# Performance work log

Hardware: AMD Instinct MI355X
Metric: run time of the kernel (lower is better)

Reference implementation:

```python
import jax, jax.numpy as jnp
import numpy as np

PS = 7        # patch (window) size
DIM = 192     # channels
HEADS = 8
HID = 768     # mlp hidden = 4*dim
B = 8
HH = 112
WW = 112
EPS = 1e-5


def _rel_pos_index(ps):
    coords = np.stack(np.meshgrid(np.arange(ps), np.arange(ps), indexing='ij'))
    cf = coords.reshape(2, -1)
    rel = (cf[:, :, None] - cf[:, None, :]).transpose(1, 2, 0).astype(np.int64)
    rel[:, :, 0] += ps - 1
    rel[:, :, 1] += ps - 1
    rel[:, :, 0] *= 2 * ps - 1
    return rel.sum(-1)  # (N, N)

REL_IDX = jnp.asarray(_rel_pos_index(PS))  # (49, 49) int


def layer_norm(x, g, b):
    m = jnp.mean(x, axis=-1, keepdims=True)
    v = jnp.var(x, axis=-1, keepdims=True)
    return (x - m) * jax.lax.rsqrt(v + EPS) * g + b


def setup_inputs() -> dict:
    key = jax.random.key(0)
    ks = jax.random.split(key, 8)
    s = 0.02
    return {
        'x': jax.random.normal(ks[0], (B, HH * WW, DIM), jnp.float32),
        'norm1_g': jnp.ones((DIM,), jnp.float32),
        'norm1_b': jnp.zeros((DIM,), jnp.float32),
        'q_w': jax.random.normal(ks[1], (DIM, DIM), jnp.float32) * s,
        'q_b': jnp.zeros((DIM,), jnp.float32),
        'kv_w': jax.random.normal(ks[2], (2 * DIM, DIM), jnp.float32) * s,
        'kv_b': jnp.zeros((2 * DIM,), jnp.float32),
        'rpe_table': jax.random.normal(ks[3], ((2 * PS - 1) ** 2, HEADS), jnp.float32) * s,
        'proj_w': jax.random.normal(ks[4], (DIM, DIM), jnp.float32) * s,
        'proj_b': jnp.zeros((DIM,), jnp.float32),
        'norm2_g': jnp.ones((DIM,), jnp.float32),
        'norm2_b': jnp.zeros((DIM,), jnp.float32),
        'fc1_w': jax.random.normal(ks[5], (HID, DIM), jnp.float32) * s,
        'fc1_b': jnp.zeros((HID,), jnp.float32),
        'dw_w': jax.random.normal(ks[6], (HID, 1, 3, 3), jnp.float32) * s,
        'dw_b': jnp.zeros((HID,), jnp.float32),
        'fc2_w': jax.random.normal(ks[7], (DIM, HID), jnp.float32) * s,
        'fc2_b': jnp.zeros((DIM,), jnp.float32),
        'H': HH,
        'W': WW,
    }


def reference(x, norm1_g, norm1_b, q_w, q_b, kv_w, kv_b, rpe_table,
              proj_w, proj_b, norm2_g, norm2_b, fc1_w, fc1_b, dw_w, dw_b,
              fc2_w, fc2_b, H, W):
    Bsz, L, C = x.shape
    N = PS * PS
    hd = C // HEADS
    scale = hd ** -0.5
    nh, nw = H // PS, W // PS  # H, W chosen divisible by PS -> no padding

    shortcut = x
    xn = layer_norm(x, norm1_g, norm1_b)
    xi = xn.reshape(Bsz, H, W, C)
    # partition into non-overlapping PS x PS windows: (B*nP, N, C)
    p = xi.reshape(Bsz, nh, PS, nw, PS, C).transpose(0, 1, 3, 2, 4, 5).reshape(-1, N, C)

    # IPSA window attention (memory == x, T = 1)
    q = (p @ q_w.T + q_b).reshape(-1, N, HEADS, hd).transpose(0, 2, 1, 3) * scale
    kv = (p @ kv_w.T + kv_b).reshape(-1, N, 2, HEADS, hd).transpose(2, 0, 3, 1, 4)
    k, v = kv[0], kv[1]  # (B_, heads, N, hd)
    attn = jnp.einsum('bhnd,bhmd->bhnm', q, k)
    bias = rpe_table[REL_IDX.reshape(-1)].reshape(N, N, HEADS).transpose(2, 0, 1)
    attn = jax.nn.softmax(attn + bias[None], axis=-1)
    out = jnp.einsum('bhnm,bhmd->bhnd', attn, v).transpose(0, 2, 1, 3).reshape(-1, N, C)
    out = out @ proj_w.T + proj_b
    # reverse window partition back to (B, L, C)
    out = out.reshape(Bsz, nh, nw, PS, PS, C).transpose(0, 1, 3, 2, 4, 5).reshape(Bsz, L, C)
    x = shortcut + out

    # MLP with depthwise conv
    y = layer_norm(x, norm2_g, norm2_b)
    y = y @ fc1_w.T + fc1_b  # (B, L, HID)
    yc = y.transpose(0, 2, 1).reshape(Bsz, HID, H, W)
    yc = jax.lax.conv_general_dilated(
        yc, dw_w, window_strides=(1, 1), padding=((1, 1), (1, 1)),
        dimension_numbers=('NCHW', 'OIHW', 'NCHW'), feature_group_count=HID,
    ) + dw_b[None, :, None, None]
    y = yc.reshape(Bsz, HID, L).transpose(0, 2, 1)
    y = jax.nn.gelu(y, approximate=False)
    y = y @ fc2_w.T + fc2_b
    return x + y
```

## Files before the change

kernel.cpp:

```cpp
#include <hip/hip_runtime.h>
#include <hip/hip_bf16.h>
#include <cmath>

#define C_DIM 192
#define HID 768

typedef __attribute__((ext_vector_type(8))) __bf16 bf16x8;
typedef __attribute__((ext_vector_type(4))) float f32x4;
typedef __attribute__((ext_vector_type(2))) float f32x2;

__device__ __forceinline__ void gload_lds16(const void* g, void* l) {
  __builtin_amdgcn_global_load_lds(
      (__attribute__((address_space(1))) void*)(const_cast<void*>(g)),
      (__attribute__((address_space(3))) void*)(l), 16, 0, 0);
}

__device__ __forceinline__ float bfu2f(ushort u) {
  return __uint_as_float((unsigned)u << 16);
}
__device__ __forceinline__ ushort f2bfu(float f) {
  __hip_bfloat16 h = __float2bfloat16(f);
  return *reinterpret_cast<ushort*>(&h);
}
__device__ __forceinline__ float fgelu(float x) {
  float z = x * (1.5957691216f + 0.071354816f * x * x);
  return x / (1.f + __expf(-z));
}

__global__ __launch_bounds__(256) void prep_kernel(
    const float* __restrict__ q_w, const float* __restrict__ q_b,
    const float* __restrict__ kv_w, const float* __restrict__ kv_b,
    const float* __restrict__ proj_w, const float* __restrict__ fc1_w,
    const float* __restrict__ fc2_w,
    __hip_bfloat16* __restrict__ wcat, float* __restrict__ bcat,
    __hip_bfloat16* __restrict__ projw, __hip_bfloat16* __restrict__ fc1w,
    __hip_bfloat16* __restrict__ fc2w)
{
  int idx = blockIdx.x * 256 + threadIdx.x;
  const float scale = 0.20412414523193154f;
  if (idx < 110592) {
    float v = (idx < 36864) ? q_w[idx] * scale : kv_w[idx - 36864];
    wcat[idx] = __float2bfloat16(v);
  }
  if (idx < 576) bcat[idx] = (idx < 192) ? q_b[idx] * scale : kv_b[idx - 192];
  if (idx < 36864) projw[idx] = __float2bfloat16(proj_w[idx]);
  if (idx < 147456) {
    fc1w[idx] = __float2bfloat16(fc1_w[idx]);
    fc2w[idx] = __float2bfloat16(fc2_w[idx]);
  }
}

__global__ __launch_bounds__(256) void ln_kernel(
    const float* __restrict__ x, const float* __restrict__ g,
    const float* __restrict__ b, __hip_bfloat16* __restrict__ out)
{
  int t = blockIdx.x * 4 + (threadIdx.x >> 6);
  int lane = threadIdx.x & 63;
  const float* xr = x + (size_t)t * C_DIM;
  float v0 = xr[lane], v1 = xr[lane + 64], v2 = xr[lane + 128];
  float s = v0 + v1 + v2;
  float sq = v0 * v0 + v1 * v1 + v2 * v2;
  #pragma unroll
  for (int off = 32; off > 0; off >>= 1) {
    s += __shfl_xor(s, off, 64);
    sq += __shfl_xor(sq, off, 64);
  }
  float mean = s * (1.0f / 192.0f);
  float var = sq * (1.0f / 192.0f) - mean * mean;
  float rstd = rsqrtf(var + 1e-5f);
  size_t o = (size_t)t * C_DIM;
  out[o + lane]       = __float2bfloat16((v0 - mean) * rstd * g[lane] + b[lane]);
  out[o + lane + 64]  = __float2bfloat16((v1 - mean) * rstd * g[lane + 64] + b[lane + 64]);
  out[o + lane + 128] = __float2bfloat16((v2 - mean) * rstd * g[lane + 128] + b[lane + 128]);
}

template <int EPI>
__global__ __launch_bounds__(512, 4) void gemmA_kernel(
    const ushort* __restrict__ X, int lda, const ushort* __restrict__ W,
    const float* __restrict__ bias, const float* __restrict__ addin,
    void* __restrict__ outp, int N)
{
  __shared__ __align__(16) ushort Al[128 * 192];
  __shared__ __align__(16) ushort Bl[64 * 192];
  const int tid = threadIdx.x;
  const int wv = tid >> 6;
  const int lane = tid & 63;
  const int quad = lane >> 4;
  const int m15 = lane & 15;
  const long mBase = (long)blockIdx.y * 128;
  const int NT = N >> 6;

  #pragma unroll
  for (int r = 0; r < 6; ++r) {
    int sI = tid + r * 512;
    int row = sI / 24;
    int cs = sI - row * 24;
    int gc = cs - (row % 24); if (gc < 0) gc += 24;
    gload_lds16(X + (mBase + row) * (long)lda + gc * 8, Al + sI * 8);
  }

  const int rA0 = wv * 16 + m15;
  const int rA0m = rA0 % 24;

  for (int nt = 0; nt < NT; ++nt) {
    __syncthreads();
    #pragma unroll
    for (int r = 0; r < 3; ++r) {
      int sI = tid + r * 512;
      int row = sI / 24;
      int cs = sI - row * 24;
      int gc = cs - (row % 24); if (gc < 0) gc += 24;
      gload_lds16(W + (long)(nt * 64 + row) * 192 + gc * 8, Bl + sI * 8);
    }
    __syncthreads();

    f32x4 acc[4];
    #pragma unroll
    for (int c = 0; c < 4; ++c) acc[c] = (f32x4){0.f, 0.f, 0.f, 0.f};

    #pragma unroll
    for (int ks = 0; ks < 6; ++ks) {
      const int l = ks * 4 + quad;
      int pa0 = l + rA0m; if (pa0 >= 24) pa0 -= 24;
      bf16x8 a0 = *(const bf16x8*)&Al[rA0 * 192 + pa0 * 8];
      #pragma unroll
      for (int ct = 0; ct < 4; ++ct) {
        const int rB = ct * 16 + m15;
        int pb = l + (rB % 24); if (pb >= 24) pb -= 24;
        bf16x8 b = *(const bf16x8*)&Bl[rB * 192 + pb * 8];
        acc[ct] = __builtin_amdgcn_mfma_f32_16x16x32_bf16(a0, b, acc[ct], 0, 0, 0);
      }
    }
    #pragma unroll
    for (int ct = 0; ct < 4; ++ct)
      #pragma unroll
      for (int i = 0; i < 4; ++i) {
        long row = mBase + wv * 16 + quad * 4 + i;
        int col = nt * 64 + ct * 16 + m15;
        float v = acc[ct][i] + bias[col];
        if (EPI == 1) {
          v += addin[row * N + col];
          ((float*)outp)[row * N + col] = v;
        } else {
          ((__hip_bfloat16*)outp)[row * N + col] = __float2bfloat16(v);
        }
      }
  }
}

__global__ __launch_bounds__(512, 4) void gemmA_ln_kernel(
    const ushort* __restrict__ X, int lda, const ushort* __restrict__ W,
    const float* __restrict__ bias, const float* __restrict__ addin,
    float* __restrict__ outp, const float* __restrict__ lng,
    const float* __restrict__ lnb, __hip_bfloat16* __restrict__ xnout)
{
  __shared__ __align__(16) ushort Al[128 * 192];
  __shared__ __align__(16) ushort Bl[64 * 192];
  const int tid = threadIdx.x;
  const int wv = tid >> 6;
  const int lane = tid & 63;
  const int quad = lane >> 4;
  const int m15 = lane & 15;
  const long mBase = (long)blockIdx.y * 128;

  #pragma unroll
  for (int r = 0; r < 6; ++r) {
    int sI = tid + r * 512;
    int row = sI / 24;
    int cs = sI - row * 24;
    int gc = cs - (row % 24); if (gc < 0) gc += 24;
    gload_lds16(X + (mBase + row) * (long)lda + gc * 8, Al + sI * 8);
  }

  const int rA0 = wv * 16 + m15;
  const int rA0m = rA0 % 24;

  f32x4 acc[3][4];
  #pragma unroll
  for (int n = 0; n < 3; ++n)
    #pragma unroll
    for (int c = 0; c < 4; ++c) acc[n][c] = (f32x4){0.f, 0.f, 0.f, 0.f};

  #pragma unroll
  for (int nt = 0; nt < 3; ++nt) {
    __syncthreads();
    #pragma unroll
    for (int r = 0; r < 3; ++r) {
      int sI = tid + r * 512;
      int row = sI / 24;
      int cs = sI - row * 24;
      int gc = cs - (row % 24); if (gc < 0) gc += 24;
      gload_lds16(W + (long)(nt * 64 + row) * 192 + gc * 8, Bl + sI * 8);
    }
    __syncthreads();
    #pragma unroll
    for (int ks = 0; ks < 6; ++ks) {
      const int l = ks * 4 + quad;
      int pa0 = l + rA0m; if (pa0 >= 24) pa0 -= 24;
      bf16x8 a0 = *(const bf16x8*)&Al[rA0 * 192 + pa0 * 8];
      #pragma unroll
      for (int ct = 0; ct < 4; ++ct) {
        const int rB = ct * 16 + m15;
        int pb = l + (rB % 24); if (pb >= 24) pb -= 24;
        bf16x8 b = *(const bf16x8*)&Bl[rB * 192 + pb * 8];
        acc[nt][ct] = __builtin_amdgcn_mfma_f32_16x16x32_bf16(a0, b, acc[nt][ct], 0, 0, 0);
      }
    }
  }

  float sum_[4], sq_[4];
  #pragma unroll
  for (int i = 0; i < 4; ++i) { sum_[i] = 0.f; sq_[i] = 0.f; }

  #pragma unroll
  for (int nt = 0; nt < 3; ++nt)
    #pragma unroll
    for (int ct = 0; ct < 4; ++ct) {
      int col = nt * 64 + ct * 16 + m15;
      float cb = bias[col];
      #pragma unroll
      for (int i = 0; i < 4; ++i) {
        long row = mBase + wv * 16 + quad * 4 + i;
        float v = acc[nt][ct][i] + cb + addin[row * 192 + col];
        outp[row * 192 + col] = v;
        acc[nt][ct][i] = v;
        sum_[i] += v;
        sq_[i] += v * v;
      }
    }

  float mean_[4], rstd_[4];
  #pragma unroll
  for (int i = 0; i < 4; ++i) {
    float s = sum_[i], q = sq_[i];
    #pragma unroll
    for (int m = 1; m < 16; m <<= 1) {
      s += __shfl_xor(s, m, 64);
      q += __shfl_xor(q, m, 64);
    }
    float mean = s * (1.0f / 192.0f);
    mean_[i] = mean;
    rstd_[i] = rsqrtf(q * (1.0f / 192.0f) - mean * mean + 1e-5f);
  }

  #pragma unroll
  for (int nt = 0; nt < 3; ++nt)
    #pragma unroll
    for (int ct = 0; ct < 4; ++ct) {
      int col = nt * 64 + ct * 16 + m15;
      float cg = lng[col], cbb = lnb[col];
      #pragma unroll
      for (int i = 0; i < 4; ++i) {
        long row = mBase + wv * 16 + quad * 4 + i;
        float v = (acc[nt][ct][i] - mean_[i]) * rstd_[i] * cg + cbb;
        xnout[row * 192 + col] = __float2bfloat16(v);
      }
    }
}

__global__ __launch_bounds__(512, 4) void gemmB_kernel(
    const ushort* __restrict__ X, const ushort* __restrict__ W,
    const float* __restrict__ bias, const float* __restrict__ addin,
    float* __restrict__ outp)
{
  __shared__ __align__(16) ushort Al[128 * 192];
  __shared__ __align__(16) ushort Bl[64 * 192];
  const int tid = threadIdx.x;
  const int wv = tid >> 6;
  const int lane = tid & 63;
  const int quad = lane >> 4;
  const int m15 = lane & 15;
  const long mBase = (long)blockIdx.y * 128;

  const int rA0 = wv * 16 + m15;
  const int rA0m = rA0 % 24;

  f32x4 acc[3][4];
  #pragma unroll
  for (int n = 0; n < 3; ++n)
    #pragma unroll
    for (int c = 0; c < 4; ++c) acc[n][c] = (f32x4){0.f, 0.f, 0.f, 0.f};

  for (int kc = 0; kc < 4; ++kc) {
    for (int nt = 0; nt < 3; ++nt) {
      __syncthreads();
      if (nt == 0) {
        #pragma unroll
        for (int r = 0; r < 6; ++r) {
          int sI = tid + r * 512;
          int row = sI / 24;
          int cs = sI - row * 24;
          int gc = cs - (row % 24); if (gc < 0) gc += 24;
          gload_lds16(X + (mBase + row) * 768l + kc * 192 + gc * 8, Al + sI * 8);
        }
      }
      #pragma unroll
      for (int r = 0; r < 3; ++r) {
        int sI = tid + r * 512;
        int row = sI / 24;
        int cs = sI - row * 24;
        int gc = cs - (row % 24); if (gc < 0) gc += 24;
        gload_lds16(W + (long)(nt * 64 + row) * 768 + kc * 192 + gc * 8, Bl + sI * 8);
      }
      __syncthreads();
      #pragma unroll
      for (int ks = 0; ks < 6; ++ks) {
        const int l = ks * 4 + quad;
        int pa0 = l + rA0m; if (pa0 >= 24) pa0 -= 24;
        bf16x8 a0 = *(const bf16x8*)&Al[rA0 * 192 + pa0 * 8];
        #pragma unroll
        for (int ct = 0; ct < 4; ++ct) {
          const int rB = ct * 16 + m15;
          int pb = l + (rB % 24); if (pb >= 24) pb -= 24;
          bf16x8 b = *(const bf16x8*)&Bl[rB * 192 + pb * 8];
          acc[nt][ct] = __builtin_amdgcn_mfma_f32_16x16x32_bf16(a0, b, acc[nt][ct], 0, 0, 0);
        }
      }
    }
  }
  #pragma unroll
  for (int nt = 0; nt < 3; ++nt)
    #pragma unroll
    for (int ct = 0; ct < 4; ++ct)
      #pragma unroll
      for (int i = 0; i < 4; ++i) {
        long row = mBase + wv * 16 + quad * 4 + i;
        int col = nt * 64 + ct * 16 + m15;
        float v = acc[nt][ct][i] + bias[col] + addin[row * 192 + col];
        outp[row * 192 + col] = v;
      }
}

__global__ __launch_bounds__(256) void attn_kernel(
    const float* __restrict__ rpe, __hip_bfloat16* __restrict__ qkv)
{
  __shared__ float lds[4 * 2352 + 4 * 172];
  const int tid = threadIdx.x;
  const int lane = tid & 63;
  const int wv = tid >> 6;
  const int wh = blockIdx.x * 4 + wv;
  const int h = wh & 7;
  const int win = wh >> 3;
  const int b = win >> 8;
  const int wl = win & 255;
  const int whi = wl >> 4;
  const int wwi = wl & 15;
  ushort* qkv_u = (ushort*)qkv;
  float* kv_w = &lds[wv * 2352];
  float* bias_w = &lds[4 * 2352 + wv * 172];

  const long rowbase = (long)b * 12544 + (long)(whi * 7) * 112 + wwi * 7;

  #pragma unroll
  for (int rnd = 0; rnd < 10; ++rnd) {
    int e = lane + rnd * 64;
    if (e < 588) {
      int t = e / 12;
      int r = e - t * 12;
      int mat = r / 6;
      int d4 = (r - mat * 6) * 4;
      int py = t / 7, px = t - py * 7;
      long row = rowbase + py * 112 + px;
      ushort4 u = *(const ushort4*)(qkv_u + row * 576 + 192 + mat * 192 + h * 24 + d4);
      float* dst = kv_w + mat * 1176 + t * 24 + d4;
      dst[0] = bfu2f(u.x); dst[1] = bfu2f(u.y);
      dst[2] = bfu2f(u.z); dst[3] = bfu2f(u.w);
    }
  }
  for (int r = lane; r < 169; r += 64) bias_w[r] = rpe[r * 8 + h];
  __syncthreads();

  const int i = (lane < 49) ? lane : 48;
  const int yi = i / 7, xi = i - yi * 7;
  const int base_i = yi * 13 + xi + 84;
  const long myrow = rowbase + yi * 112 + xi;

  f32x2 q2[12];
  #pragma unroll
  for (int d4 = 0; d4 < 24; d4 += 4) {
    ushort4 u = *(const ushort4*)(qkv_u + myrow * 576 + h * 24 + d4);
    q2[(d4 >> 1)]     = (f32x2){bfu2f(u.x), bfu2f(u.y)};
    q2[(d4 >> 1) + 1] = (f32x2){bfu2f(u.z), bfu2f(u.w)};
  }

  float s[49];
  #pragma unroll
  for (int j = 0; j < 49; ++j) {
    const int yj = j / 7, xj = j % 7;
    const int base_j = yj * 13 + xj;
    const float* kr = kv_w + j * 24;
    f32x2 a2 = {0.f, 0.f};
    #pragma unroll
    for (int d4 = 0; d4 < 24; d4 += 4) {
      f32x4 kk = *(const f32x4*)(kr + d4);
      f32x2 klo = __builtin_shufflevector(kk, kk, 0, 1);
      f32x2 khi = __builtin_shufflevector(kk, kk, 2, 3);
      a2 += q2[(d4 >> 1)] * klo;
      a2 += q2[(d4 >> 1) + 1] * khi;
    }
    s[j] = a2[0] + a2[1] + bias_w[base_i - base_j];
  }

  float m0 = fmaxf(s[0], s[48]);
  float m1 = s[1], m2 = s[2], m3 = s[3];
  #pragma unroll
  for (int j = 4; j < 48; j += 4) {
    m0 = fmaxf(m0, s[j]);     m1 = fmaxf(m1, s[j + 1]);
    m2 = fmaxf(m2, s[j + 2]); m3 = fmaxf(m3, s[j + 3]);
  }
  const float mx = fmaxf(fmaxf(m0, m1), fmaxf(m2, m3));

  #pragma unroll
  for (int j = 0; j < 49; ++j) s[j] = __expf(s[j] - mx);

  float t0 = s[48], t1 = 0.f, t2 = 0.f, t3 = 0.f;
  #pragma unroll
  for (int j = 0; j < 48; j += 4) {
    t0 += s[j]; t1 += s[j + 1]; t2 += s[j + 2]; t3 += s[j + 3];
  }
  const float inv = 1.f / ((t0 + t1) + (t2 + t3));
  #pragma unroll
  for (int j = 0; j < 49; ++j) s[j] *= inv;

  f32x2 o2[12];
  #pragma unroll
  for (int dd = 0; dd < 12; ++dd) o2[dd] = (f32x2){0.f, 0.f};
  #pragma unroll
  for (int j = 0; j < 49; ++j) {
    const f32x2 p2 = {s[j], s[j]};
    const float* vr = kv_w + 1176 + j * 24;
    #pragma unroll
    for (int d4 = 0; d4 < 24; d4 += 4) {
      f32x4 vv = *(const f32x4*)(vr + d4);
      o2[(d4 >> 1)]     += p2 * __builtin_shufflevector(vv, vv, 0, 1);
      o2[(d4 >> 1) + 1] += p2 * __builtin_shufflevector(vv, vv, 2, 3);
    }
  }

  if (lane < 49) {
    #pragma unroll
    for (int d4 = 0; d4 < 24; d4 += 4) {
      ushort4 u;
      u.x = f2bfu(o2[(d4 >> 1)][0]);     u.y = f2bfu(o2[(d4 >> 1)][1]);
      u.z = f2bfu(o2[(d4 >> 1) + 1][0]); u.w = f2bfu(o2[(d4 >> 1) + 1][1]);
      *(ushort4*)(qkv_u + myrow * 576 + h * 24 + d4) = u;
    }
  }
}

__global__ __launch_bounds__(192) void dwconv_gelu_kernel(
    const ushort* __restrict__ y1, const float* __restrict__ w,
    const float* __restrict__ bias, ushort* __restrict__ y2)
{
  const int c = threadIdx.x * 4;
  const int w0 = blockIdx.y * 2;
  const int b = blockIdx.z;
  const int h0 = blockIdx.x * 28;

  float wt[9][4];
  #pragma unroll
  for (int k = 0; k < 9; ++k)
    #pragma unroll
    for (int j = 0; j < 4; ++j) wt[k][j] = w[(c + j) * 9 + k];
  float bs[4];
  #pragma unroll
  for (int j = 0; j < 4; ++j) bs[j] = bias[c + j];

  const bool okL = (w0 > 0), okR = (w0 + 2 < 112);
  ushort4 rb[6][4];

  auto loadrow = [&](int h, ushort4 dst[4]) {
    const ushort4 z = {0, 0, 0, 0};
    if (h < 0 || h >= 112) {
      dst[0] = z; dst[1] = z; dst[2] = z; dst[3] = z;
      return;
    }
    const ushort* p = y1 + (((size_t)(b * 112 + h)) * 112 + w0) * HID + c;
    dst[0] = okL ? *(const ushort4*)(p - HID) : z;
    dst[1] = *(const ushort4*)(p);
    dst[2] = *(const ushort4*)(p + HID);
    dst[3] = okR ? *(const ushort4*)(p + 2 * HID) : z;
  };

  loadrow(h0 - 1, rb[0]);
  loadrow(h0, rb[1]);

  for (int m = 0; m < 7; ++m) {
    const int hb = h0 + m * 4;
    loadrow(hb + 1, rb[2]);
    loadrow(hb + 2, rb[3]);
    loadrow(hb + 3, rb[4]);
    loadrow(hb + 4, rb[5]);
    #pragma unroll
    for (int o = 0; o < 4; ++o) {
      float acc0[4], acc1[4];
      #pragma unroll
      for (int j = 0; j < 4; ++j) { acc0[j] = bs[j]; acc1[j] = bs[j]; }
      #pragma unroll
      for (int dy = 0; dy < 3; ++dy) {
        float col[4][4];
        #pragma unroll
        for (int x = 0; x < 4; ++x) {
          ushort4 u = rb[o + dy][x];
          col[x][0] = bfu2f(u.x); col[x][1] = bfu2f(u.y);
          col[x][2] = bfu2f(u.z); col[x][3] = bfu2f(u.w);
        }
        #pragma unroll
        for (int dx = 0; dx < 3; ++dx)
          #pragma unroll
          for (int j = 0; j < 4; ++j) {
            acc0[j] += wt[dy * 3 + dx][j] * col[dx][j];
            acc1[j] += wt[dy * 3 + dx][j] * col[dx + 1][j];
          }
      }
      ushort* outp = y2 + (((size_t)(b * 112 + hb + o)) * 112 + w0) * HID + c;
      ushort4 o0, o1;
      o0.x = f2bfu(fgelu(acc0[0])); o0.y = f2bfu(fgelu(acc0[1]));
      o0.z = f2bfu(fgelu(acc0[2])); o0.w = f2bfu(fgelu(acc0[3]));
      o1.x = f2bfu(fgelu(acc1[0])); o1.y = f2bfu(fgelu(acc1[1]));
      o1.z = f2bfu(fgelu(acc1[2])); o1.w = f2bfu(fgelu(acc1[3]));
      *(ushort4*)(outp) = o0;
      *(ushort4*)(outp + HID) = o1;
    }
    #pragma unroll
    for (int x = 0; x < 4; ++x) {
      rb[0][x] = rb[4][x];
      rb[1][x] = rb[5][x];
    }
  }
}

extern "C" void kernel_launch(void* const* d_in, const int* in_sizes, int n_in,
                              void* d_out, int out_size, void* d_ws, size_t ws_size,
                              hipStream_t stream) {
  const float* x      = (const float*)d_in[0];
  const float* n1g    = (const float*)d_in[1];
  const float* n1b    = (const float*)d_in[2];
  const float* q_w    = (const float*)d_in[3];
  const float* q_b    = (const float*)d_in[4];
  const float* kv_w   = (const float*)d_in[5];
  const float* kv_b   = (const float*)d_in[6];
  const float* rpe    = (const float*)d_in[7];
  const float* proj_w = (const float*)d_in[8];
  const float* proj_b = (const float*)d_in[9];
  const float* n2g    = (const float*)d_in[10];
  const float* n2b    = (const float*)d_in[11];
  const float* fc1_w  = (const float*)d_in[12];
  const float* fc1_b  = (const float*)d_in[13];
  const float* dw_w   = (const float*)d_in[14];
  const float* dw_b   = (const float*)d_in[15];
  const float* fc2_w  = (const float*)d_in[16];
  const float* fc2_b  = (const float*)d_in[17];
  float* out = (float*)d_out;

  char* ws = (char*)d_ws;
  __hip_bfloat16* wcat  = (__hip_bfloat16*)(ws);
  __hip_bfloat16* projw = (__hip_bfloat16*)(ws + 221184);
  __hip_bfloat16* fc1w  = (__hip_bfloat16*)(ws + 294912);
  __hip_bfloat16* fc2w  = (__hip_bfloat16*)(ws + 589824);
  float* bcat           = (float*)(ws + 884736);
  const size_t WOFF = 1u << 20;

  int CB = 8;
  while (CB > 1 && WOFF + (size_t)CB * 12544 * 3456 > ws_size) CB >>= 1;
  const size_t Mc = (size_t)CB * 12544;
  char* Abuf = ws + WOFF;
  char* Bbuf = Abuf + Mc * 384;
  char* Cbuf = Bbuf + Mc * 1536;
  __hip_bfloat16* xn  = (__hip_bfloat16*)Abuf;
  __hip_bfloat16* qkv = (__hip_bfloat16*)Bbuf;
  __hip_bfloat16* y2  = (__hip_bfloat16*)Bbuf;
  __hip_bfloat16* y1  = (__hip_bfloat16*)Cbuf;

  prep_kernel<<<576, 256, 0, stream>>>(q_w, q_b, kv_w, kv_b, proj_w, fc1_w,
                                       fc2_w, wcat, bcat, projw, fc1w, fc2w);

  const int nChunks = 8 / CB;
  const int mt = CB * 98;
  for (int cchunk = 0; cchunk < nChunks; ++cchunk) {
    const size_t toff = (size_t)cchunk * Mc;
    const float* xc = x + toff * C_DIM;
    float* oc = out + toff * C_DIM;

    ln_kernel<<<(int)(Mc / 4), 256, 0, stream>>>(xc, n1g, n1b, xn);
    gemmA_kernel<0><<<dim3(1, mt), 512, 0, stream>>>(
        (const ushort*)xn, 192, (const ushort*)wcat, bcat, nullptr, qkv, 576);
    attn_kernel<<<CB * 512, 256, 0, stream>>>(rpe, qkv);
    gemmA_ln_kernel<<<dim3(1, mt), 512, 0, stream>>>(
        (const ushort*)qkv, 576, (const ushort*)projw, proj_b, xc, oc,
        n2g, n2b, xn);
    gemmA_kernel<0><<<dim3(1, mt), 512, 0, stream>>>(
        (const ushort*)xn, 192, (const ushort*)fc1w, fc1_b, nullptr, y1, 768);
    dwconv_gelu_kernel<<<dim3(4, 56, CB), 192, 0, stream>>>(
        (const ushort*)y1, dw_w, dw_b, (ushort*)y2);
    gemmB_kernel<<<dim3(1, mt), 512, 0, stream>>>(
        (const ushort*)y2, (const ushort*)fc2w, fc2_b, oc, oc);
  }
}
```

Before: 629.2 us.

## Rewrite window attention kernel to use MFMA for QK^T and PV

Replaces the per-lane scalar fp32 dot products in the window attention kernel with bf16 MFMA 16x16x32 instructions for both the score and output products. Q and K fragments are loaded straight from global memory, V and the probability matrix are staged in swizzled LDS, and softmax reduces across lanes with shuffles. It also sets an occupancy hint in the launch bounds. The aim is to cut the ALU and LDS traffic of the scalar loops, at the cost of padding 49 tokens to 64 and holding probabilities in bf16, which lowers precision.

```diff
diff --git a/kernel.cpp b/kernel.cpp
--- a/kernel.cpp
+++ b/kernel.cpp
@@ -8,6 +8,8 @@
 typedef __attribute__((ext_vector_type(8))) __bf16 bf16x8;
 typedef __attribute__((ext_vector_type(4))) float f32x4;
 typedef __attribute__((ext_vector_type(2))) float f32x2;
+typedef __attribute__((ext_vector_type(8))) unsigned short u16x8;
+typedef __attribute__((ext_vector_type(4))) unsigned int u32x4;
 
 __device__ __forceinline__ void gload_lds16(const void* g, void* l) {
   __builtin_amdgcn_global_load_lds(
@@ -331,13 +333,15 @@
       }
 }
 
-__global__ __launch_bounds__(256) void attn_kernel(
+__global__ __launch_bounds__(256, 3) void attn_kernel(
     const float* __restrict__ rpe, __hip_bfloat16* __restrict__ qkv)
 {
-  __shared__ float lds[4 * 2352 + 4 * 172];
+  __shared__ __align__(16) char smem[51968];
   const int tid = threadIdx.x;
   const int lane = tid & 63;
   const int wv = tid >> 6;
+  const int quad = lane >> 4;
+  const int m15 = lane & 15;
   const int wh = blockIdx.x * 4 + wv;
   const int h = wh & 7;
   const int win = wh >> 3;
@@ -346,106 +350,178 @@
   const int whi = wl >> 4;
   const int wwi = wl & 15;
   ushort* qkv_u = (ushort*)qkv;
-  float* kv_w = &lds[wv * 2352];
-  float* bias_w = &lds[4 * 2352 + wv * 172];
+  char* Vb = smem + wv * 4096;
+  char* Pb = smem + 16384 + wv * 8192;
+  float* biasW = (float*)(smem + 49152 + wv * 704);
 
   const long rowbase = (long)b * 12544 + (long)(whi * 7) * 112 + wwi * 7;
 
-  #pragma unroll
-  for (int rnd = 0; rnd < 10; ++rnd) {
-    int e = lane + rnd * 64;
-    if (e < 588) {
-      int t = e / 12;
-      int r = e - t * 12;
-      int mat = r / 6;
-      int d4 = (r - mat * 6) * 4;
-      int py = t / 7, px = t - py * 7;
+  {
+    int j = lane;
+    int f = ((j >> 3) & 3) << 5;
+    if (j < 49) {
+      int py = j / 7, px = j - py * 7;
       long row = rowbase + py * 112 + px;
-      ushort4 u = *(const ushort4*)(qkv_u + row * 576 + 192 + mat * 192 + h * 24 + d4);
-      float* dst = kv_w + mat * 1176 + t * 24 + d4;
-      dst[0] = bfu2f(u.x); dst[1] = bfu2f(u.y);
-      dst[2] = bfu2f(u.z); dst[3] = bfu2f(u.w);
-    }
-  }
-  for (int r = lane; r < 169; r += 64) bias_w[r] = rpe[r * 8 + h];
-  __syncthreads();
-
-  const int i = (lane < 49) ? lane : 48;
-  const int yi = i / 7, xi = i - yi * 7;
-  const int base_i = yi * 13 + xi + 84;
-  const long myrow = rowbase + yi * 112 + xi;
-
-  f32x2 q2[12];
-  #pragma unroll
-  for (int d4 = 0; d4 < 24; d4 += 4) {
-    ushort4 u = *(const ushort4*)(qkv_u + myrow * 576 + h * 24 + d4);
-    q2[(d4 >> 1)]     = (f32x2){bfu2f(u.x), bfu2f(u.y)};
-    q2[(d4 >> 1) + 1] = (f32x2){bfu2f(u.z), bfu2f(u.w)};
-  }
-
-  float s[49];
-  #pragma unroll
-  for (int j = 0; j < 49; ++j) {
-    const int yj = j / 7, xj = j % 7;
-    const int base_j = yj * 13 + xj;
-    const float* kr = kv_w + j * 24;
-    f32x2 a2 = {0.f, 0.f};
-    #pragma unroll
-    for (int d4 = 0; d4 < 24; d4 += 4) {
-      f32x4 kk = *(const f32x4*)(kr + d4);
-      f32x2 klo = __builtin_shufflevector(kk, kk, 0, 1);
-      f32x2 khi = __builtin_shufflevector(kk, kk, 2, 3);
-      a2 += q2[(d4 >> 1)] * klo;
-      a2 += q2[(d4 >> 1) + 1] * khi;
-    }
-    s[j] = a2[0] + a2[1] + bias_w[base_i - base_j];
-  }
-
-  float m0 = fmaxf(s[0], s[48]);
-  float m1 = s[1], m2 = s[2], m3 = s[3];
-  #pragma unroll
-  for (int j = 4; j < 48; j += 4) {
-    m0 = fmaxf(m0, s[j]);     m1 = fmaxf(m1, s[j + 1]);
-    m2 = fmaxf(m2, s[j + 2]); m3 = fmaxf(m3, s[j + 3]);
-  }
-  const float mx = fmaxf(fmaxf(m0, m1), fmaxf(m2, m3));
-
-  #pragma unroll
-  for (int j = 0; j < 49; ++j) s[j] = __expf(s[j] - mx);
-
-  float t0 = s[48], t1 = 0.f, t2 = 0.f, t3 = 0.f;
-  #pragma unroll
-  for (int j = 0; j < 48; j += 4) {
-    t0 += s[j]; t1 += s[j + 1]; t2 += s[j + 2]; t3 += s[j + 3];
-  }
-  const float inv = 1.f / ((t0 + t1) + (t2 + t3));
-  #pragma unroll
-  for (int j = 0; j < 49; ++j) s[j] *= inv;
-
-  f32x2 o2[12];
-  #pragma unroll
-  for (int dd = 0; dd < 12; ++dd) o2[dd] = (f32x2){0.f, 0.f};
-  #pragma unroll
-  for (int j = 0; j < 49; ++j) {
-    const f32x2 p2 = {s[j], s[j]};
-    const float* vr = kv_w + 1176 + j * 24;
-    #pragma unroll
-    for (int d4 = 0; d4 < 24; d4 += 4) {
-      f32x4 vv = *(const f32x4*)(vr + d4);
-      o2[(d4 >> 1)]     += p2 * __builtin_shufflevector(vv, vv, 0, 1);
-      o2[(d4 >> 1) + 1] += p2 * __builtin_shufflevector(vv, vv, 2, 3);
-    }
-  }
-
-  if (lane < 49) {
-    #pragma unroll
-    for (int d4 = 0; d4 < 24; d4 += 4) {
-      ushort4 u;
-      u.x = f2bfu(o2[(d4 >> 1)][0]);     u.y = f2bfu(o2[(d4 >> 1)][1]);
-      u.z = f2bfu(o2[(d4 >> 1) + 1][0]); u.w = f2bfu(o2[(d4 >> 1) + 1][1]);
-      *(ushort4*)(qkv_u + myrow * 576 + h * 24 + d4) = u;
-    }
-  }
+      const ushort* src = qkv_u + row * 576 + 384 + h * 24;
+      #pragma unroll
+      for (int c = 0; c < 3; ++c) {
+        u16x8 val = *(const u16x8*)(src + c * 8);
+        *(u16x8*)(Vb + ((j * 64 + c * 16) ^ f)) = val;
+      }
+    } else {
+      u16x8 z = {};
+      #pragma unroll
+      for (int c = 0; c < 4; ++c)
+        *(u16x8*)(Vb + ((j * 64 + c * 16) ^ f)) = z;
+    }
+  }
+  for (int r = lane; r < 169; r += 64) biasW[r] = rpe[r * 8 + h];
+
+  int bi[4];
+  #pragma unroll
+  for (int rt = 0; rt < 4; ++rt) {
+    int r = rt * 16 + m15; if (r > 48) r = 48;
+    bi[rt] = (r / 7) * 13 + (r % 7) + 84;
+  }
+  int bj4[4][4];
+  #pragma unroll
+  for (int jt = 0; jt < 4; ++jt)
+    #pragma unroll
+    for (int i = 0; i < 4; ++i) {
+      int j = jt * 16 + quad * 4 + i; if (j > 48) j = 48;
+      bj4[jt][i] = (j / 7) * 13 + (j % 7);
+    }
+
+  f32x4 sacc[4][4];
+  #pragma unroll
+  for (int jt = 0; jt < 4; ++jt)
+    #pragma unroll
+    for (int rt = 0; rt < 4; ++rt)
+      #pragma unroll
+      for (int i = 0; i < 4; ++i)
+        sacc[jt][rt][i] = biasW[bi[rt] - bj4[jt][i]];
+
+  bf16x8 kf[4], qf[4];
+  const bf16x8 zf = {};
+  #pragma unroll
+  for (int jt = 0; jt < 4; ++jt) {
+    int t = jt * 16 + m15; if (t > 48) t = 48;
+    long row = rowbase + (t / 7) * 112 + (t % 7);
+    kf[jt] = *(const bf16x8*)(qkv_u + row * 576 + 192 + h * 24 + quad * 8);
+    if (quad == 3) kf[jt] = zf;
+  }
+  #pragma unroll
+  for (int rt = 0; rt < 4; ++rt) {
+    int t = rt * 16 + m15; if (t > 48) t = 48;
+    long row = rowbase + (t / 7) * 112 + (t % 7);
+    qf[rt] = *(const bf16x8*)(qkv_u + row * 576 + h * 24 + quad * 8);
+  }
+  #pragma unroll
+  for (int jt = 0; jt < 4; ++jt)
+    #pragma unroll
+    for (int rt = 0; rt < 4; ++rt)
+      sacc[jt][rt] = __builtin_amdgcn_mfma_f32_16x16x32_bf16(
+          kf[jt], qf[rt], sacc[jt][rt], 0, 0, 0);
+
+  #pragma unroll
+  for (int rt = 0; rt < 4; ++rt) {
+    if (quad != 0) sacc[3][rt][0] = -1e30f;
+    sacc[3][rt][1] = -1e30f;
+    sacc[3][rt][2] = -1e30f;
+    sacc[3][rt][3] = -1e30f;
+  }
+
+  float inv[4];
+  #pragma unroll
+  for (int rt = 0; rt < 4; ++rt) {
+    float mx = sacc[0][rt][0];
+    #pragma unroll
+    for (int jt = 0; jt < 4; ++jt)
+      #pragma unroll
+      for (int i = 0; i < 4; ++i)
+        mx = fmaxf(mx, sacc[jt][rt][i]);
+    mx = fmaxf(mx, __shfl_xor(mx, 16, 64));
+    mx = fmaxf(mx, __shfl_xor(mx, 32, 64));
+    float sum = 0.f;
+    #pragma unroll
+    for (int jt = 0; jt < 4; ++jt)
+      #pragma unroll
+      for (int i = 0; i < 4; ++i) {
+        float p = __expf(sacc[jt][rt][i] - mx);
+        sacc[jt][rt][i] = p;
+        sum += p;
+      }
+    sum += __shfl_xor(sum, 16, 64);
+    sum += __shfl_xor(sum, 32, 64);
+    inv[rt] = 1.f / sum;
+  }
+
+  const int swzP = (m15 & 7) << 4;
+  #pragma unroll
+  for (int rt = 0; rt < 4; ++rt)
+    #pragma unroll
+    for (int jt = 0; jt < 4; ++jt)
+      #pragma unroll
+      for (int u = 0; u < 2; ++u) {
+        unsigned pk;
+        asm("v_cvt_pk_bf16_f32 %0, %1, %2"
+            : "=v"(pk)
+            : "v"(sacc[jt][rt][2 * u]), "v"(sacc[jt][rt][2 * u + 1]));
+        int j0 = jt * 16 + quad * 4 + 2 * u;
+        int lin = (rt * 16 + m15) * 128 + j0 * 2;
+        *(unsigned*)(Pb + (lin ^ swzP)) = pk;
+      }
+
+  f32x4 oacc[4][2];
+  #pragma unroll
+  for (int mt = 0; mt < 4; ++mt)
+    #pragma unroll
+    for (int nt = 0; nt < 2; ++nt) oacc[mt][nt] = (f32x4){0.f, 0.f, 0.f, 0.f};
+
+  #pragma unroll
+  for (int kt = 0; kt < 2; ++kt) {
+    bf16x8 pf[4];
+    #pragma unroll
+    for (int mt = 0; mt < 4; ++mt) {
+      int lin = (mt * 16 + m15) * 128 + kt * 64 + quad * 16;
+      pf[mt] = *(const bf16x8*)(Pb + (lin ^ swzP));
+    }
+    bf16x8 vf[2];
+    #pragma unroll
+    for (int nt = 0; nt < 2; ++nt) {
+      u32x4 w;
+      #pragma unroll
+      for (int e2 = 0; e2 < 4; ++e2) {
+        int j_lo = kt * 32 + quad * 8 + 2 * e2;
+        int lin_lo = j_lo * 64 + (nt * 16 + m15) * 2;
+        int lin_hi = lin_lo + 64;
+        unsigned lo = *(const ushort*)(Vb + (lin_lo ^ (quad << 5)));
+        unsigned hi = *(const ushort*)(Vb + (lin_hi ^ (quad << 5)));
+        w[e2] = lo | (hi << 16);
+      }
+      vf[nt] = __builtin_bit_cast(bf16x8, w);
+    }
+    #pragma unroll
+    for (int mt = 0; mt < 4; ++mt)
+      #pragma unroll
+      for (int nt = 0; nt < 2; ++nt)
+        oacc[mt][nt] = __builtin_amdgcn_mfma_f32_16x16x32_bf16(
+            pf[mt], vf[nt], oacc[mt][nt], 0, 0, 0);
+  }
+
+  #pragma unroll
+  for (int mt = 0; mt < 4; ++mt)
+    #pragma unroll
+    for (int i = 0; i < 4; ++i) {
+      float iv = __shfl(inv[mt], quad * 4 + i, 64);
+      int r = mt * 16 + quad * 4 + i;
+      if (r < 49) {
+        long row = rowbase + (r / 7) * 112 + (r % 7);
+        ushort* dst = qkv_u + row * 576 + h * 24;
+        dst[m15] = f2bfu(oacc[mt][0][i] * iv);
+        if (m15 < 8) dst[16 + m15] = f2bfu(oacc[mt][1][i] * iv);
+      }
+    }
 }
 
 __global__ __launch_bounds__(192) void dwconv_gelu_kernel(
```

Measured after the change: 587.2 us. 6.7% less time.
